# Performance work log

Measured on AMD Instinct MI355X. Metric: run time of the kernel, lower is better.

Reference implementation:

```python
import jax, jax.numpy as jnp
import numpy as np

B, C, H, W = 8, 2, 512, 512  # features hard-coded to 2 by Conv3x3(2,1)
N_ATTN = 6  # 3 ResidualAttentionUnits x 2 AttentionConv each
HALF = C // 2


def _conv1x1(x, w, b):
    # x: [B,C,H,W], w: [O,C], b: [O]
    return jnp.einsum('bchw,oc->bohw', x, w) + b[None, :, None, None]


def _unfold3(x):
    # x: [B,C,H+2,W+2] -> [B,C,H,W,3,3] (height-window, width-window), matching
    # torch unfold(2,3,1).unfold(3,3,1)
    Hh = x.shape[2] - 2
    Ww = x.shape[3] - 2
    return jnp.stack(
        [jnp.stack([x[:, :, i:i + Hh, j:j + Ww] for j in range(3)], axis=-1)
         for i in range(3)], axis=-2)


def _attn_conv(x, wq, bq, wk, bk, wv, bv, rh, rw):
    # Local 3x3 window self-attention (AttentionConv, groups=1).
    b_, c_, h_, w_ = x.shape
    xp = jnp.pad(x, ((0, 0), (0, 0), (1, 1), (1, 1)))  # zero pad=1
    q = _conv1x1(x, wq, bq)                 # [B,Co,H,W]
    k = _unfold3(_conv1x1(xp, wk, bk))      # [B,Co,H,W,3,3]
    v = _unfold3(_conv1x1(xp, wv, bv))
    co = q.shape[1]
    half = co // 2
    # rh, rw: [half,3]; rel_h broadcast over kh, rel_w over kw
    k = jnp.concatenate([
        k[:, :half] + rh[None, :, None, None, :, None],
        k[:, half:] + rw[None, :, None, None, None, :]], axis=1)
    k = k.reshape(b_, co, h_, w_, 9)
    v = v.reshape(b_, co, h_, w_, 9)
    attn = jax.nn.softmax(q[..., None] * k, axis=-1)  # softmax over 9 window positions
    return jnp.einsum('bchwk,bchwk->bchw', attn, v)


def _rau(x, p, u):
    # ResidualAttentionUnit: relu -> atten1 -> relu -> atten2 -> +x
    wq, bq, wk, bk, wv, bv, rh, rw = p
    i, j = 2 * u, 2 * u + 1
    h = jax.nn.relu(x)
    h = _attn_conv(h, wq[i], bq[i], wk[i], bk[i], wv[i], bv[i], rh[i], rw[i])
    h = jax.nn.relu(h)
    h = _attn_conv(h, wq[j], bq[j], wk[j], bk[j], wv[j], bv[j], rh[j], rw[j])
    return h + x


def _up2_bilinear_ac(x):
    # bilinear, scale_factor=2, align_corners=True
    b_, c_, h_, w_ = x.shape
    ho, wo = 2 * h_, 2 * w_
    ys = jnp.linspace(0.0, h_ - 1.0, ho)
    xs = jnp.linspace(0.0, w_ - 1.0, wo)
    y0 = jnp.floor(ys).astype(jnp.int32)
    x0 = jnp.floor(xs).astype(jnp.int32)
    y1 = jnp.clip(y0 + 1, 0, h_ - 1)
    x1 = jnp.clip(x0 + 1, 0, w_ - 1)
    wy = (ys - y0)[None, None, :, None]
    wx = (xs - x0)[None, None, None, :]
    r0 = x[:, :, y0, :]
    r1 = x[:, :, y1, :]
    v00 = r0[:, :, :, x0]
    v01 = r0[:, :, :, x1]
    v10 = r1[:, :, :, x0]
    v11 = r1[:, :, :, x1]
    return (v00 * (1 - wy) * (1 - wx) + v01 * (1 - wy) * wx
            + v10 * wy * (1 - wx) + v11 * wy * wx)


def _forward(input_1, input_2, wq, bq, wk, bk, wv, bv, rh, rw, conv_w, conv_b):
    p = (wq, bq, wk, bk, wv, bv, rh, rw)
    out = _rau(input_1, p, 0) + _rau(input_2, p, 1)
    out = _rau(out, p, 2)
    xp = jnp.pad(out, ((0, 0), (0, 0), (1, 1), (1, 1)), mode='reflect')
    out = jax.lax.conv_general_dilated(
        xp, conv_w, (1, 1), 'VALID',
        dimension_numbers=('NCHW', 'OIHW', 'NCHW')) + conv_b[None, :, None, None]
    out = jax.nn.sigmoid(out)
    return out, _up2_bilinear_ac(out)


def setup_inputs() -> dict:
    key = jax.random.key(0)
    ks = jax.random.split(key, 12)
    return {
        'input_1': jax.random.normal(ks[0], (B, C, H, W), jnp.float32),
        'input_2': jax.random.normal(ks[1], (B, C, H, W), jnp.float32),
        # stacked params for the 6 AttentionConv modules (all bias=True)
        'wq': jax.random.normal(ks[2], (N_ATTN, C, C), jnp.float32) * 0.5,
        'bq': jax.random.normal(ks[3], (N_ATTN, C), jnp.float32) * 0.1,
        'wk': jax.random.normal(ks[4], (N_ATTN, C, C), jnp.float32) * 0.5,
        'bk': jax.random.normal(ks[5], (N_ATTN, C), jnp.float32) * 0.1,
        'wv': jax.random.normal(ks[6], (N_ATTN, C, C), jnp.float32) * 0.5,
        'bv': jax.random.normal(ks[7], (N_ATTN, C), jnp.float32) * 0.1,
        'rh': jax.random.normal(ks[8], (N_ATTN, HALF, 3), jnp.float32),
        'rw': jax.random.normal(ks[9], (N_ATTN, HALF, 3), jnp.float32),
        # Conv3x3(2,1): reflection-pad + 3x3 conv
        'conv_w': jax.random.normal(ks[10], (1, 2, 3, 3), jnp.float32) * 0.2,
        'conv_b': jax.random.normal(ks[11], (1,), jnp.float32) * 0.1,
    }


def reference(input_1, input_2, wq, bq, wk, bk, wv, bv, rh, rw, conv_w, conv_b):
    return _forward(input_1, input_2, wq, bq, wk, bk, wv, bv, rh, rw, conv_w, conv_b)
```

## Files before the change

kernel.cpp:

```cpp
#include <hip/hip_runtime.h>

#if __has_builtin(__builtin_amdgcn_exp2f)
#define EXP2F(x) __builtin_amdgcn_exp2f(x)
#else
#define EXP2F(x) exp2f(x)
#endif

typedef float v2f __attribute__((ext_vector_type(2)));
typedef _Float16 h2v __attribute__((ext_vector_type(2)));
typedef _Float16 h4v __attribute__((ext_vector_type(4)));

constexpr int B = 8, H = 512, W = 512;
constexpr int PLANE = H * W;
constexpr int BSTRIDE = 2 * PLANE;
constexpr int NPIX = B * PLANE;
constexpr int PPITCH = 520;
constexpr int PXOFF  = 4;
constexpr int PPLANE = H * PPITCH;
constexpr int PBUF   = 16 * PPLANE;
constexpr float LOG2E = 1.4426950408889634f;

__device__ __forceinline__ float reluf(float v) { return v > 0.f ? v : 0.f; }
__device__ __forceinline__ float frcp(float v) { return __builtin_amdgcn_rcpf(v); }
__device__ __forceinline__ v2f vfma(v2f a, v2f b, v2f c) { return __builtin_elementwise_fma(a, b, c); }
__device__ __forceinline__ v2f vmax2(v2f a, v2f b) { return __builtin_elementwise_max(a, b); }
__device__ __forceinline__ v2f bc(float x) { v2f r; r.x = x; r.y = x; return r; }

__device__ __forceinline__ unsigned swz8(unsigned bid, unsigned nwg)
{
    return (bid & 7u) * (nwg >> 3) + (bid >> 3);
}

struct AttnW {
    v2f wq0, wq1, bq;
    v2f wk0, wk1;
    v2f biasK[3];
    float rwL[3];
    v2f wv0, wv1, bv;
};

__device__ __forceinline__ AttnW load_w(
    const float* wq, const float* bq, const float* wk, const float* bk,
    const float* wv, const float* bv, const float* rh, const float* rw, int i)
{
    AttnW P;
    P.wq0.x = wq[4*i];   P.wq0.y = wq[4*i+2];
    P.wq1.x = wq[4*i+1]; P.wq1.y = wq[4*i+3];
    P.bq.x  = bq[2*i];   P.bq.y  = bq[2*i+1];
    P.wk0.x = wk[4*i]   * LOG2E; P.wk0.y = wk[4*i+2] * LOG2E;
    P.wk1.x = wk[4*i+1] * LOG2E; P.wk1.y = wk[4*i+3] * LOG2E;
    float bk1L = bk[2*i+1] * LOG2E;
#pragma unroll
    for (int r = 0; r < 3; ++r) {
        P.biasK[r].x = (bk[2*i] + rh[3*i+r]) * LOG2E;
        P.biasK[r].y = bk1L;
    }
#pragma unroll
    for (int d = 0; d < 3; ++d) P.rwL[d] = rw[3*i+d] * LOG2E;
    P.wv0.x = wv[4*i];   P.wv0.y = wv[4*i+2];
    P.wv1.x = wv[4*i+1]; P.wv1.y = wv[4*i+3];
    P.bv.x  = bv[2*i];   P.bv.y  = bv[2*i+1];
    return P;
}

__device__ __forceinline__ void attn_strip(
    const v2f (&t)[3][6], const AttnW& P, v2f (&o)[4])
{
    v2f kk[3][6], vv[3][6];
#pragma unroll
    for (int r = 0; r < 3; ++r)
#pragma unroll
        for (int c = 0; c < 6; ++c) {
            v2f u0 = bc(t[r][c].x), u1 = bc(t[r][c].y);
            kk[r][c] = vfma(P.wk0, u0, vfma(P.wk1, u1, P.biasK[r]));
            vv[r][c] = vfma(P.wv0, u0, vfma(P.wv1, u1, P.bv));
        }
#pragma unroll
    for (int px = 0; px < 4; ++px) {
        v2f q = vfma(P.wq0, bc(t[1][px+1].x), vfma(P.wq1, bc(t[1][px+1].y), P.bq));
        v2f addv[3];
#pragma unroll
        for (int d = 0; d < 3; ++d) { addv[d].x = 0.f; addv[d].y = q.y * P.rwL[d]; }
        v2f s[9];
#pragma unroll
        for (int r = 0; r < 3; ++r)
#pragma unroll
            for (int d = 0; d < 3; ++d)
                s[r*3+d] = vfma(q, kk[r][px+d], addv[d]);
        v2f m = vmax2(vmax2(vmax2(vmax2(s[0], s[1]), vmax2(s[2], s[3])),
                            vmax2(vmax2(s[4], s[5]), vmax2(s[6], s[7]))), s[8]);
        v2f sum = bc(0.f), acc = bc(0.f);
#pragma unroll
        for (int r = 0; r < 3; ++r)
#pragma unroll
            for (int d = 0; d < 3; ++d) {
                v2f dd = s[r*3+d] - m;
                v2f e; e.x = EXP2F(dd.x); e.y = EXP2F(dd.y);
                sum += e;
                acc = vfma(e, vv[r][px+d], acc);
            }
        v2f rs; rs.x = frcp(sum.x); rs.y = frcp(sum.y);
        o[px] = acc * rs;
    }
}


__device__ __forceinline__ void store_padded_h(
    _Float16* outp, int b2, int y, int x0, const v2f (&o)[4])
{
    int ob = b2 * PPLANE + y * PPITCH + x0 + PXOFF;
    h4v h0, h1;
    h0.x = (_Float16)o[0].x; h0.y = (_Float16)o[1].x; h0.z = (_Float16)o[2].x; h0.w = (_Float16)o[3].x;
    h1.x = (_Float16)o[0].y; h1.y = (_Float16)o[1].y; h1.z = (_Float16)o[2].y; h1.w = (_Float16)o[3].y;
    *reinterpret_cast<h4v*>(outp + ob)          = h0;
    *reinterpret_cast<h4v*>(outp + ob + PPLANE) = h1;
    if (x0 == 0 || x0 == W - 4) {
        h4v z; z.x = z.y = z.z = z.w = (_Float16)0.f;
        int pb = b2 * PPLANE + y * PPITCH + (x0 == 0 ? 0 : PXOFF + W);
        *reinterpret_cast<h4v*>(outp + pb)          = z;
        *reinterpret_cast<h4v*>(outp + pb + PPLANE) = z;
    }
}

__device__ __forceinline__ void load_t_padded_h(
    unsigned s, const _Float16* __restrict__ xp, v2f (&t)[3][6])
{
    int x0 = (s & 127) * 4;
    int y  = (s >> 7) & 511;
    int b  = s >> 16;

    const _Float16* xb0 = xp + (b * 2) * PPLANE + x0 + PXOFF;
#pragma unroll
    for (int r = 0; r < 3; ++r) {
        int gy = y - 1 + r;
        bool ok = (unsigned)gy < (unsigned)H;
        int gyc = ok ? gy : y;
        const _Float16* p0 = xb0 + gyc * PPITCH;
        const _Float16* p1 = p0 + PPLANE;
        h2v a0 = *reinterpret_cast<const h2v*>(p0 - 2);
        h2v a1 = *reinterpret_cast<const h2v*>(p0);
        h2v a2 = *reinterpret_cast<const h2v*>(p0 + 2);
        h2v a3 = *reinterpret_cast<const h2v*>(p0 + 4);
        h2v c0 = *reinterpret_cast<const h2v*>(p1 - 2);
        h2v c1 = *reinterpret_cast<const h2v*>(p1);
        h2v c2 = *reinterpret_cast<const h2v*>(p1 + 2);
        h2v c3 = *reinterpret_cast<const h2v*>(p1 + 4);
        if (ok) {
            t[r][0].x = reluf((float)a0.y); t[r][0].y = reluf((float)c0.y);
            t[r][1].x = reluf((float)a1.x); t[r][1].y = reluf((float)c1.x);
            t[r][2].x = reluf((float)a1.y); t[r][2].y = reluf((float)c1.y);
            t[r][3].x = reluf((float)a2.x); t[r][3].y = reluf((float)c2.x);
            t[r][4].x = reluf((float)a2.y); t[r][4].y = reluf((float)c2.y);
            t[r][5].x = reluf((float)a3.x); t[r][5].y = reluf((float)c3.x);
        } else {
#pragma unroll
            for (int c = 0; c < 6; ++c) { t[r][c].x = 0.f; t[r][c].y = 0.f; }
        }
    }
}

__device__ __forceinline__ void load_t_unpadded(
    unsigned s, const float* __restrict__ x, v2f (&t)[3][6])
{
    int x0 = (s & 127) * 4;
    int y  = (s >> 7) & 511;
    int b  = s >> 16;

    const float* xb = x + b * BSTRIDE;
    bool rowv[3] = { y > 0, true, y < H - 1 };
    int  yr[3]   = { y > 0 ? y - 1 : 0, y, y < H - 1 ? y + 1 : H - 1 };
    bool lv   = x0 > 0;
    bool rvld = x0 < W - 4;
    int  xl = lv ? x0 - 1 : 0;
    int  xr = rvld ? x0 + 4 : W - 1;

#pragma unroll
    for (int r = 0; r < 3; ++r) {
        const float* p0 = xb + yr[r] * W;
        const float* p1 = p0 + PLANE;
        float4 a0 = *reinterpret_cast<const float4*>(p0 + x0);
        float4 a1 = *reinterpret_cast<const float4*>(p1 + x0);
        float u0[6] = { p0[xl], a0.x, a0.y, a0.z, a0.w, p0[xr] };
        float u1[6] = { p1[xl], a1.x, a1.y, a1.z, a1.w, p1[xr] };
        bool rv_ = rowv[r];
#pragma unroll
        for (int c = 0; c < 6; ++c) {
            bool ok = rv_ && (c > 0 || lv) && (c < 5 || rvld);
            t[r][c].x = ok ? reluf(u0[c]) : 0.f;
            t[r][c].y = ok ? reluf(u1[c]) : 0.f;
        }
    }
}


__global__ __launch_bounds__(256) void attn_in_kernel(
    const float* __restrict__ xA, const float* __restrict__ xB,
    _Float16* outA, _Float16* outB,
    const float* __restrict__ wq, const float* __restrict__ bq,
    const float* __restrict__ wk, const float* __restrict__ bk,
    const float* __restrict__ wv, const float* __restrict__ bv,
    const float* __restrict__ rh, const float* __restrict__ rw,
    int piA, int piB)
{
    unsigned wid = swz8(blockIdx.x, 4096);
    bool second = wid >= 2048;
    AttnW P = load_w(wq, bq, wk, bk, wv, bv, rh, rw, second ? piB : piA);
    unsigned s = (second ? wid - 2048 : wid) * 256u + threadIdx.x;

    v2f t[3][6];
    load_t_unpadded(s, second ? xB : xA, t);
    v2f o[4];
    attn_strip(t, P, o);

    store_padded_h(second ? outB : outA, (s >> 16) * 2, (s >> 7) & 511, (s & 127) * 4, o);
}

__global__ __launch_bounds__(256) void attn_fused23_kernel(
    const _Float16* __restrict__ A, const _Float16* __restrict__ Bb,
    const float* __restrict__ in1, const float* __restrict__ in2,
    _Float16* __restrict__ C,
    const float* __restrict__ wq, const float* __restrict__ bq,
    const float* __restrict__ wk, const float* __restrict__ bk,
    const float* __restrict__ wv, const float* __restrict__ bv,
    const float* __restrict__ rh, const float* __restrict__ rw)
{
    unsigned s = swz8(blockIdx.x, 2048) * 256u + threadIdx.x;
    int x0 = (s & 127) * 4;
    int y  = (s >> 7) & 511;
    int b  = s >> 16;
    int base0 = b * BSTRIDE + y * W + x0;
    int base1 = base0 + PLANE;

    v2f t[3][6];
    v2f o1[4], o2[4];

    {
        AttnW P1 = load_w(wq, bq, wk, bk, wv, bv, rh, rw, 1);
        load_t_padded_h(s, A, t);
        attn_strip(t, P1, o1);
        float4 ra = *reinterpret_cast<const float4*>(in1 + base0);
        float4 rb = *reinterpret_cast<const float4*>(in1 + base1);
        o1[0].x += ra.x; o1[1].x += ra.y; o1[2].x += ra.z; o1[3].x += ra.w;
        o1[0].y += rb.x; o1[1].y += rb.y; o1[2].y += rb.z; o1[3].y += rb.w;
    }
    {
        AttnW P3 = load_w(wq, bq, wk, bk, wv, bv, rh, rw, 3);
        load_t_padded_h(s, Bb, t);
        attn_strip(t, P3, o2);
        float4 ra = *reinterpret_cast<const float4*>(in2 + base0);
        float4 rb = *reinterpret_cast<const float4*>(in2 + base1);
        o2[0].x += ra.x + o1[0].x; o2[1].x += ra.y + o1[1].x;
        o2[2].x += ra.z + o1[2].x; o2[3].x += ra.w + o1[3].x;
        o2[0].y += rb.x + o1[0].y; o2[1].y += rb.y + o1[1].y;
        o2[2].y += rb.z + o1[2].y; o2[3].y += rb.w + o1[3].y;
    }

    store_padded_h(C, b * 2, y, x0, o2);
}

__global__ __launch_bounds__(256) void attn4_kernel(
    const _Float16* __restrict__ C, _Float16* __restrict__ Bb,
    const float* __restrict__ wq, const float* __restrict__ bq,
    const float* __restrict__ wk, const float* __restrict__ bk,
    const float* __restrict__ wv, const float* __restrict__ bv,
    const float* __restrict__ rh, const float* __restrict__ rw)
{
    unsigned s = swz8(blockIdx.x, 2048) * 256u + threadIdx.x;
    AttnW P = load_w(wq, bq, wk, bk, wv, bv, rh, rw, 4);
    v2f t[3][6];
    load_t_padded_h(s, C, t);
    v2f o[4];
    attn_strip(t, P, o);
    store_padded_h(Bb, (s >> 16) * 2, (s >> 7) & 511, (s & 127) * 4, o);
}

__global__ __launch_bounds__(256) void attn5_kernel(
    const _Float16* __restrict__ Bb, _Float16* __restrict__ C,
    const float* __restrict__ wq, const float* __restrict__ bq,
    const float* __restrict__ wk, const float* __restrict__ bk,
    const float* __restrict__ wv, const float* __restrict__ bv,
    const float* __restrict__ rh, const float* __restrict__ rw)
{
    unsigned s = swz8(blockIdx.x, 2048) * 256u + threadIdx.x;
    AttnW P = load_w(wq, bq, wk, bk, wv, bv, rh, rw, 5);
    v2f t[3][6];
    load_t_padded_h(s, Bb, t);
    v2f o[4];
    attn_strip(t, P, o);

    int x0 = (s & 127) * 4;
    int y  = (s >> 7) & 511;
    int b  = s >> 16;
    int ob = (b * 2) * PPLANE + y * PPITCH + x0 + PXOFF;
    h4v r0 = *reinterpret_cast<const h4v*>(C + ob);
    h4v r1 = *reinterpret_cast<const h4v*>(C + ob + PPLANE);
    o[0].x += (float)r0.x; o[1].x += (float)r0.y; o[2].x += (float)r0.z; o[3].x += (float)r0.w;
    o[0].y += (float)r1.x; o[1].y += (float)r1.y; o[2].y += (float)r1.z; o[3].y += (float)r1.w;

    h4v h0, h1;
    h0.x = (_Float16)o[0].x; h0.y = (_Float16)o[1].x; h0.z = (_Float16)o[2].x; h0.w = (_Float16)o[3].x;
    h1.x = (_Float16)o[0].y; h1.y = (_Float16)o[1].y; h1.z = (_Float16)o[2].y; h1.w = (_Float16)o[3].y;
    *reinterpret_cast<h4v*>(C + ob)          = h0;
    *reinterpret_cast<h4v*>(C + ob + PPLANE) = h1;
}

__global__ __launch_bounds__(256) void conv_sig4_kernel(
    const _Float16* __restrict__ u,
    const float* __restrict__ cw, const float* __restrict__ cb,
    float* __restrict__ o)
{
    unsigned s = swz8(blockIdx.x, 2048) * 256u + threadIdx.x;
    int x0 = (s & 127) * 4;
    int y  = (s >> 7) & 511;
    int b  = s >> 16;

    float w[18];
#pragma unroll
    for (int i = 0; i < 18; ++i) w[i] = cw[i];

    int yy[3];
#pragma unroll
    for (int i = 0; i < 3; ++i) {
        int t = y + i - 1;
        if (t < 0) t = -t;
        if (t > H - 1) t = 2 * (H - 1) - t;
        yy[i] = t;
    }
    int xl = x0 - 1; if (xl < 0) xl = 1;
    int xr = x0 + 4; if (xr > W - 1) xr = 2 * (W - 1) - xr;

    float acc[4] = { cb[0], cb[0], cb[0], cb[0] };
#pragma unroll
    for (int c = 0; c < 2; ++c) {
        const _Float16* up = u + (b * 2 + c) * PPLANE + PXOFF;
#pragma unroll
        for (int i = 0; i < 3; ++i) {
            const _Float16* row = up + yy[i] * PPITCH;
            h2v m0 = *reinterpret_cast<const h2v*>(row + x0);
            h2v m1 = *reinterpret_cast<const h2v*>(row + x0 + 2);
            float t6[6] = { (float)row[xl], (float)m0.x, (float)m0.y,
                            (float)m1.x, (float)m1.y, (float)row[xr] };
#pragma unroll
            for (int j = 0; j < 3; ++j) {
                float wc = w[c * 9 + i * 3 + j];
#pragma unroll
                for (int px = 0; px < 4; ++px)
                    acc[px] = fmaf(t6[px + j], wc, acc[px]);
            }
        }
    }
    float4 ov;
    ov.x = frcp(1.f + EXP2F(-acc[0] * LOG2E));
    ov.y = frcp(1.f + EXP2F(-acc[1] * LOG2E));
    ov.z = frcp(1.f + EXP2F(-acc[2] * LOG2E));
    ov.w = frcp(1.f + EXP2F(-acc[3] * LOG2E));
    *reinterpret_cast<float4*>(o + b * PLANE + y * W + x0) = ov;
}

__global__ __launch_bounds__(256) void upsample4_kernel(
    const float* __restrict__ o, float* __restrict__ up)
{
    unsigned p = swz8(blockIdx.x, 8192) * 256u + threadIdx.x;
    int b  = p >> 18;
    int y  = (p >> 8) & 1023;
    int x0 = (p & 255) * 4;

    const float scale = 511.0f / 1023.0f;
    float fy = y * scale;
    int y0 = (int)fy;
    float wy = fy - y0;
    int y1 = min(y0 + 1, H - 1);

    const float* ob = o + b * PLANE;
    const float* row0 = ob + y0 * W;
    const float* row1 = ob + y1 * W;

    float4 ov;
    float* ovp = &ov.x;
#pragma unroll
    for (int j = 0; j < 4; ++j) {
        float fx = (x0 + j) * scale;
        int xi = (int)fx;
        float wx = fx - xi;
        int xi1 = min(xi + 1, W - 1);
        float v00 = row0[xi], v01 = row0[xi1];
        float v10 = row1[xi], v11 = row1[xi1];
        float top = fmaf(v01 - v00, wx, v00);
        float bot = fmaf(v11 - v10, wx, v10);
        ovp[j] = fmaf(bot - top, wy, top);
    }
    *reinterpret_cast<float4*>(up + ((long)b << 20) + y * 1024 + x0) = ov;
}

extern "C" void kernel_launch(void* const* d_in, const int* in_sizes, int n_in,
                              void* d_out, int out_size, void* d_ws, size_t ws_size,
                              hipStream_t stream) {
    const float* in1 = (const float*)d_in[0];
    const float* in2 = (const float*)d_in[1];
    const float* wq  = (const float*)d_in[2];
    const float* bq  = (const float*)d_in[3];
    const float* wk  = (const float*)d_in[4];
    const float* bk  = (const float*)d_in[5];
    const float* wv  = (const float*)d_in[6];
    const float* bv  = (const float*)d_in[7];
    const float* rh  = (const float*)d_in[8];
    const float* rw  = (const float*)d_in[9];
    const float* cw  = (const float*)d_in[10];
    const float* cb  = (const float*)d_in[11];

    float* out = (float*)d_out;
    _Float16* A  = (_Float16*)out;
    _Float16* Bb = (_Float16*)out + PBUF;
    _Float16* C  = (_Float16*)d_ws;
    (void)ws_size; (void)out_size; (void)n_in; (void)in_sizes;

    dim3 blk(256);

    attn_in_kernel<<<4096, blk, 0, stream>>>(in1, in2, A, Bb,
        wq, bq, wk, bk, wv, bv, rh, rw, 0, 2);
    attn_fused23_kernel<<<2048, blk, 0, stream>>>(A, Bb, in1, in2, C,
        wq, bq, wk, bk, wv, bv, rh, rw);
    attn4_kernel<<<2048, blk, 0, stream>>>(C, Bb,
        wq, bq, wk, bk, wv, bv, rh, rw);
    attn5_kernel<<<2048, blk, 0, stream>>>(Bb, C,
        wq, bq, wk, bk, wv, bv, rh, rw);
    conv_sig4_kernel<<<2048, blk, 0, stream>>>(C, cw, cb, out);
    upsample4_kernel<<<8192, blk, 0, stream>>>(out, out + NPIX);
}
```

Before: 99.80 us.

## Merge input attention passes, precompute fp16 residual sum, move ReLU to producers

The first kernel now handles both inputs in one thread and writes an fp16 sum of the two raw inputs as the residual. This lets the fused second kernel read one half-precision residual buffer instead of two fp32 input tensors. ReLU is applied when intermediates are stored rather than on every load, and the padded fp16 loads use 4-wide vectors. The trade-offs are an extra intermediate buffer placed inside the output region, fp16 rounding of the residual sum, and a first kernel with half as many blocks but twice the work per thread.

After: 103.7 us. 1.04x slower.

```diff
diff --git a/kernel.cpp b/kernel.cpp
--- a/kernel.cpp
+++ b/kernel.cpp
@@ -105,13 +105,19 @@
 }
 
 
+template<bool RELU>
 __device__ __forceinline__ void store_padded_h(
     _Float16* outp, int b2, int y, int x0, const v2f (&o)[4])
 {
     int ob = b2 * PPLANE + y * PPITCH + x0 + PXOFF;
     h4v h0, h1;
-    h0.x = (_Float16)o[0].x; h0.y = (_Float16)o[1].x; h0.z = (_Float16)o[2].x; h0.w = (_Float16)o[3].x;
-    h1.x = (_Float16)o[0].y; h1.y = (_Float16)o[1].y; h1.z = (_Float16)o[2].y; h1.w = (_Float16)o[3].y;
+#pragma unroll
+    for (int j = 0; j < 4; ++j) {
+        float vx = RELU ? reluf(o[j].x) : o[j].x;
+        float vy = RELU ? reluf(o[j].y) : o[j].y;
+        h0[j] = (_Float16)vx;
+        h1[j] = (_Float16)vy;
+    }
     *reinterpret_cast<h4v*>(outp + ob)          = h0;
     *reinterpret_cast<h4v*>(outp + ob + PPLANE) = h1;
     if (x0 == 0 || x0 == W - 4) {
@@ -122,6 +128,7 @@
     }
 }
 
+template<bool DO_RELU>
 __device__ __forceinline__ void load_t_padded_h(
     unsigned s, const _Float16* __restrict__ xp, v2f (&t)[3][6])
 {
@@ -137,21 +144,18 @@
         int gyc = ok ? gy : y;
         const _Float16* p0 = xb0 + gyc * PPITCH;
         const _Float16* p1 = p0 + PPLANE;
-        h2v a0 = *reinterpret_cast<const h2v*>(p0 - 2);
-        h2v a1 = *reinterpret_cast<const h2v*>(p0);
-        h2v a2 = *reinterpret_cast<const h2v*>(p0 + 2);
-        h2v a3 = *reinterpret_cast<const h2v*>(p0 + 4);
-        h2v c0 = *reinterpret_cast<const h2v*>(p1 - 2);
-        h2v c1 = *reinterpret_cast<const h2v*>(p1);
-        h2v c2 = *reinterpret_cast<const h2v*>(p1 + 2);
-        h2v c3 = *reinterpret_cast<const h2v*>(p1 + 4);
+        h4v m0 = *reinterpret_cast<const h4v*>(p0);
+        h4v m1 = *reinterpret_cast<const h4v*>(p1);
+        float l0 = (float)p0[-1], r0e = (float)p0[4];
+        float l1 = (float)p1[-1], r1e = (float)p1[4];
         if (ok) {
-            t[r][0].x = reluf((float)a0.y); t[r][0].y = reluf((float)c0.y);
-            t[r][1].x = reluf((float)a1.x); t[r][1].y = reluf((float)c1.x);
-            t[r][2].x = reluf((float)a1.y); t[r][2].y = reluf((float)c1.y);
-            t[r][3].x = reluf((float)a2.x); t[r][3].y = reluf((float)c2.x);
-            t[r][4].x = reluf((float)a2.y); t[r][4].y = reluf((float)c2.y);
-            t[r][5].x = reluf((float)a3.x); t[r][5].y = reluf((float)c3.x);
+            float u0[6] = { l0, (float)m0.x, (float)m0.y, (float)m0.z, (float)m0.w, r0e };
+            float u1[6] = { l1, (float)m1.x, (float)m1.y, (float)m1.z, (float)m1.w, r1e };
+#pragma unroll
+            for (int c = 0; c < 6; ++c) {
+                t[r][c].x = DO_RELU ? reluf(u0[c]) : u0[c];
+                t[r][c].y = DO_RELU ? reluf(u1[c]) : u1[c];
+            }
         } else {
 #pragma unroll
             for (int c = 0; c < 6; ++c) { t[r][c].x = 0.f; t[r][c].y = 0.f; }
@@ -160,7 +164,8 @@
 }
 
 __device__ __forceinline__ void load_t_unpadded(
-    unsigned s, const float* __restrict__ x, v2f (&t)[3][6])
+    unsigned s, const float* __restrict__ x, v2f (&t)[3][6],
+    float4& c0raw, float4& c1raw)
 {
     int x0 = (s & 127) * 4;
     int y  = (s >> 7) & 511;
@@ -180,6 +185,7 @@
         const float* p1 = p0 + PLANE;
         float4 a0 = *reinterpret_cast<const float4*>(p0 + x0);
         float4 a1 = *reinterpret_cast<const float4*>(p1 + x0);
+        if (r == 1) { c0raw = a0; c1raw = a1; }
         float u0[6] = { p0[xl], a0.x, a0.y, a0.z, a0.w, p0[xr] };
         float u1[6] = { p1[xl], a1.x, a1.y, a1.z, a1.w, p1[xr] };
         bool rv_ = rowv[r];
@@ -194,30 +200,48 @@
 
 
 __global__ __launch_bounds__(256) void attn_in_kernel(
-    const float* __restrict__ xA, const float* __restrict__ xB,
-    _Float16* outA, _Float16* outB,
+    const float* __restrict__ in1, const float* __restrict__ in2,
+    _Float16* outA, _Float16* outB, _Float16* rsum,
     const float* __restrict__ wq, const float* __restrict__ bq,
     const float* __restrict__ wk, const float* __restrict__ bk,
     const float* __restrict__ wv, const float* __restrict__ bv,
-    const float* __restrict__ rh, const float* __restrict__ rw,
-    int piA, int piB)
-{
-    unsigned wid = swz8(blockIdx.x, 4096);
-    bool second = wid >= 2048;
-    AttnW P = load_w(wq, bq, wk, bk, wv, bv, rh, rw, second ? piB : piA);
-    unsigned s = (second ? wid - 2048 : wid) * 256u + threadIdx.x;
+    const float* __restrict__ rh, const float* __restrict__ rw)
+{
+    unsigned s = swz8(blockIdx.x, 2048) * 256u + threadIdx.x;
+    int x0 = (s & 127) * 4;
+    int y  = (s >> 7) & 511;
+    int b  = s >> 16;
 
     v2f t[3][6];
-    load_t_unpadded(s, second ? xB : xA, t);
     v2f o[4];
-    attn_strip(t, P, o);
-
-    store_padded_h(second ? outB : outA, (s >> 16) * 2, (s >> 7) & 511, (s & 127) * 4, o);
+    float4 c0a, c1a, c0b, c1b;
+
+    {
+        AttnW P0 = load_w(wq, bq, wk, bk, wv, bv, rh, rw, 0);
+        load_t_unpadded(s, in1, t, c0a, c1a);
+        attn_strip(t, P0, o);
+        store_padded_h<true>(outA, b * 2, y, x0, o);
+    }
+    {
+        AttnW P2 = load_w(wq, bq, wk, bk, wv, bv, rh, rw, 2);
+        load_t_unpadded(s, in2, t, c0b, c1b);
+        attn_strip(t, P2, o);
+        store_padded_h<true>(outB, b * 2, y, x0, o);
+    }
+
+    int base0 = b * BSTRIDE + y * W + x0;
+    h4v r0h, r1h;
+    r0h.x = (_Float16)(c0a.x + c0b.x); r0h.y = (_Float16)(c0a.y + c0b.y);
+    r0h.z = (_Float16)(c0a.z + c0b.z); r0h.w = (_Float16)(c0a.w + c0b.w);
+    r1h.x = (_Float16)(c1a.x + c1b.x); r1h.y = (_Float16)(c1a.y + c1b.y);
+    r1h.z = (_Float16)(c1a.z + c1b.z); r1h.w = (_Float16)(c1a.w + c1b.w);
+    *reinterpret_cast<h4v*>(rsum + base0)         = r0h;
+    *reinterpret_cast<h4v*>(rsum + base0 + PLANE) = r1h;
 }
 
 __global__ __launch_bounds__(256) void attn_fused23_kernel(
     const _Float16* __restrict__ A, const _Float16* __restrict__ Bb,
-    const float* __restrict__ in1, const float* __restrict__ in2,
+    const _Float16* __restrict__ rsum,
     _Float16* __restrict__ C,
     const float* __restrict__ wq, const float* __restrict__ bq,
     const float* __restrict__ wk, const float* __restrict__ bk,
@@ -228,34 +252,31 @@
     int x0 = (s & 127) * 4;
     int y  = (s >> 7) & 511;
     int b  = s >> 16;
-    int base0 = b * BSTRIDE + y * W + x0;
-    int base1 = base0 + PLANE;
 
     v2f t[3][6];
     v2f o1[4], o2[4];
 
     {
         AttnW P1 = load_w(wq, bq, wk, bk, wv, bv, rh, rw, 1);
-        load_t_padded_h(s, A, t);
+        load_t_padded_h<false>(s, A, t);
         attn_strip(t, P1, o1);
-        float4 ra = *reinterpret_cast<const float4*>(in1 + base0);
-        float4 rb = *reinterpret_cast<const float4*>(in1 + base1);
-        o1[0].x += ra.x; o1[1].x += ra.y; o1[2].x += ra.z; o1[3].x += ra.w;
-        o1[0].y += rb.x; o1[1].y += rb.y; o1[2].y += rb.z; o1[3].y += rb.w;
     }
     {
         AttnW P3 = load_w(wq, bq, wk, bk, wv, bv, rh, rw, 3);
-        load_t_padded_h(s, Bb, t);
+        load_t_padded_h<false>(s, Bb, t);
         attn_strip(t, P3, o2);
-        float4 ra = *reinterpret_cast<const float4*>(in2 + base0);
-        float4 rb = *reinterpret_cast<const float4*>(in2 + base1);
-        o2[0].x += ra.x + o1[0].x; o2[1].x += ra.y + o1[1].x;
-        o2[2].x += ra.z + o1[2].x; o2[3].x += ra.w + o1[3].x;
-        o2[0].y += rb.x + o1[0].y; o2[1].y += rb.y + o1[1].y;
-        o2[2].y += rb.z + o1[2].y; o2[3].y += rb.w + o1[3].y;
-    }
-
-    store_padded_h(C, b * 2, y, x0, o2);
+    }
+
+    int base0 = b * BSTRIDE + y * W + x0;
+    h4v r0 = *reinterpret_cast<const h4v*>(rsum + base0);
+    h4v r1 = *reinterpret_cast<const h4v*>(rsum + base0 + PLANE);
+#pragma unroll
+    for (int j = 0; j < 4; ++j) {
+        o2[j].x += o1[j].x + (float)r0[j];
+        o2[j].y += o1[j].y + (float)r1[j];
+    }
+
+    store_padded_h<false>(C, b * 2, y, x0, o2);
 }
 
 __global__ __launch_bounds__(256) void attn4_kernel(
@@ -268,10 +289,10 @@
     unsigned s = swz8(blockIdx.x, 2048) * 256u + threadIdx.x;
     AttnW P = load_w(wq, bq, wk, bk, wv, bv, rh, rw, 4);
     v2f t[3][6];
-    load_t_padded_h(s, C, t);
+    load_t_padded_h<true>(s, C, t);
     v2f o[4];
     attn_strip(t, P, o);
-    store_padded_h(Bb, (s >> 16) * 2, (s >> 7) & 511, (s & 127) * 4, o);
+    store_padded_h<true>(Bb, (s >> 16) * 2, (s >> 7) & 511, (s & 127) * 4, o);
 }
 
 __global__ __launch_bounds__(256) void attn5_kernel(
@@ -284,7 +305,7 @@
     unsigned s = swz8(blockIdx.x, 2048) * 256u + threadIdx.x;
     AttnW P = load_w(wq, bq, wk, bk, wv, bv, rh, rw, 5);
     v2f t[3][6];
-    load_t_padded_h(s, Bb, t);
+    load_t_padded_h<false>(s, Bb, t);
     v2f o[4];
     attn_strip(t, P, o);
 
@@ -294,12 +315,12 @@
     int ob = (b * 2) * PPLANE + y * PPITCH + x0 + PXOFF;
     h4v r0 = *reinterpret_cast<const h4v*>(C + ob);
     h4v r1 = *reinterpret_cast<const h4v*>(C + ob + PPLANE);
-    o[0].x += (float)r0.x; o[1].x += (float)r0.y; o[2].x += (float)r0.z; o[3].x += (float)r0.w;
-    o[0].y += (float)r1.x; o[1].y += (float)r1.y; o[2].y += (float)r1.z; o[3].y += (float)r1.w;
-
     h4v h0, h1;
-    h0.x = (_Float16)o[0].x; h0.y = (_Float16)o[1].x; h0.z = (_Float16)o[2].x; h0.w = (_Float16)o[3].x;
-    h1.x = (_Float16)o[0].y; h1.y = (_Float16)o[1].y; h1.z = (_Float16)o[2].y; h1.w = (_Float16)o[3].y;
+#pragma unroll
+    for (int j = 0; j < 4; ++j) {
+        h0[j] = (_Float16)(o[j].x + (float)r0[j]);
+        h1[j] = (_Float16)(o[j].y + (float)r1[j]);
+    }
     *reinterpret_cast<h4v*>(C + ob)          = h0;
     *reinterpret_cast<h4v*>(C + ob + PPLANE) = h1;
 }
@@ -336,10 +357,9 @@
 #pragma unroll
         for (int i = 0; i < 3; ++i) {
             const _Float16* row = up + yy[i] * PPITCH;
-            h2v m0 = *reinterpret_cast<const h2v*>(row + x0);
-            h2v m1 = *reinterpret_cast<const h2v*>(row + x0 + 2);
+            h4v m0 = *reinterpret_cast<const h4v*>(row + x0);
             float t6[6] = { (float)row[xl], (float)m0.x, (float)m0.y,
-                            (float)m1.x, (float)m1.y, (float)row[xr] };
+                            (float)m0.z, (float)m0.w, (float)row[xr] };
 #pragma unroll
             for (int j = 0; j < 3; ++j) {
                 float wc = w[c * 9 + i * 3 + j];
@@ -411,14 +431,15 @@
     float* out = (float*)d_out;
     _Float16* A  = (_Float16*)out;
     _Float16* Bb = (_Float16*)out + PBUF;
+    _Float16* R  = (_Float16*)out + 2 * PBUF;
     _Float16* C  = (_Float16*)d_ws;
     (void)ws_size; (void)out_size; (void)n_in; (void)in_sizes;
 
     dim3 blk(256);
 
-    attn_in_kernel<<<4096, blk, 0, stream>>>(in1, in2, A, Bb,
-        wq, bq, wk, bk, wv, bv, rh, rw, 0, 2);
-    attn_fused23_kernel<<<2048, blk, 0, stream>>>(A, Bb, in1, in2, C,
+    attn_in_kernel<<<2048, blk, 0, stream>>>(in1, in2, A, Bb, R,
+        wq, bq, wk, bk, wv, bv, rh, rw);
+    attn_fused23_kernel<<<2048, blk, 0, stream>>>(A, Bb, R, C,
         wq, bq, wk, bk, wv, bv, rh, rw);
     attn4_kernel<<<2048, blk, 0, stream>>>(C, Bb,
         wq, bq, wk, bk, wv, bv, rh, rw);
```
